# Kernel optimization log

Measured on AMD Instinct MI355X. Metric: run time of the kernel, lower is better.

Reference implementation:

```python
import jax, jax.numpy as jnp
import numpy as np

B, N, E, L, H, FA = 64, 29, 812, 9, 256, 5  # batch, max atoms, edges, layers, hidden, atom types
SCALE = 15.0


def _scatter_add(vals, idx):
    # vals [B,E,D], idx [B,E] -> [B,N,D]  (replaces one-hot multiply + reduce_sum)
    return jax.vmap(lambda v, i: jnp.zeros((N, v.shape[-1]), v.dtype).at[i].add(v))(vals, idx)


def _align(x, mask):
    n = jnp.sum(mask, axis=1, keepdims=True)
    mean = jnp.sum(x, axis=1, keepdims=True) / n
    return (x - mean) * mask


def setup_inputs() -> dict:
    key = jax.random.key(0)
    ks = iter(jax.random.split(key, 32))
    # fully connected edges i != j, same graph per batch element
    pairs = np.array([(i, j) for i in range(N) for j in range(N) if i != j], dtype=np.int32)
    edge_indices = jnp.tile(jnp.asarray(pairs)[None], (B, 1, 1))
    x_in = jax.random.normal(next(ks), (B, N, 3), jnp.float32)
    h_in = jax.random.normal(next(ks), (B, N, FA), jnp.float32)
    t = jax.random.uniform(next(ks), (B, N, 1), jnp.float32)
    node_mask = jnp.ones((B, N, 1), jnp.float32)
    edge_mask = jnp.ones((B, E, 1), jnp.float32)

    def w(k, shape, fan):
        return jax.random.normal(k, shape, jnp.float32) / np.float32(np.sqrt(fan))

    params = dict(
        win_w=w(next(ks), (FA + 1, H), FA + 1), win_b=jnp.zeros((H,), jnp.float32),
        wout_w=w(next(ks), (H, FA + 1), H), wout_b=jnp.zeros((FA + 1,), jnp.float32),
        e_w1=w(next(ks), (L, 2 * H + 2, H), 2 * H + 2), e_b1=jnp.zeros((L, H), jnp.float32),
        e_w2=w(next(ks), (L, H, H), H), e_b2=jnp.zeros((L, H), jnp.float32),
        att_w=w(next(ks), (L, H, 1), H), att_b=jnp.zeros((L, 1), jnp.float32),
        h_w1=w(next(ks), (L, 2 * H, H), 2 * H), h_b1=jnp.zeros((L, H), jnp.float32),
        h_w2=w(next(ks), (L, H, H), H), h_b2=jnp.zeros((L, H), jnp.float32),
        x_w1=w(next(ks), (L, 2 * H + 2, H), 2 * H + 2), x_b1=jnp.zeros((L, H), jnp.float32),
        x_w2=w(next(ks), (L, H, H), H), x_b2=jnp.zeros((L, H), jnp.float32),
        x_w3=w(next(ks), (L, H, 1), H),
    )
    return {"x_in": x_in, "h_in": h_in, "t": t, "node_mask": node_mask,
            "edge_mask": edge_mask, "edge_indices": edge_indices, **params}


def _forward(x_in, h_in, t, node_mask, edge_mask, edge_indices, p):
    bidx = jnp.arange(x_in.shape[0])[:, None]
    idx_i, idx_j = edge_indices[..., 0], edge_indices[..., 1]
    h = jnp.concatenate([h_in, t], axis=-1) @ p["win_w"] + p["win_b"]
    x = x_in
    # global pairwise distances, masked (the `a` feature)
    xi0, xj0 = x[bidx, idx_i], x[bidx, idx_j]
    a = jnp.sqrt(jnp.sum((xi0 - xj0) ** 2, axis=-1, keepdims=True)) * edge_mask
    for l in range(L):
        x_i, x_j = x[bidx, idx_i], x[bidx, idx_j]
        diff = (x_i - x_j) * edge_mask              # [B,E,3]
        d = jnp.sqrt(jnp.sum(diff ** 2, axis=-1, keepdims=True))
        h_i, h_j = h[bidx, idx_i], h[bidx, idx_j]
        feat = jnp.concatenate([h_i, h_j, d ** 2, a], axis=-1)  # [B,E,514]
        # --- update_x ---
        u = jax.nn.silu(feat @ p["x_w1"][l] + p["x_b1"][l])
        u = jax.nn.silu(u @ p["x_w2"][l] + p["x_b2"][l])
        u = jnp.tanh(u @ p["x_w3"][l]) * SCALE      # [B,E,1]
        u = u * diff / (d + 1.0)                    # [B,E,3]
        x = (x + _scatter_add(u, idx_i)) * node_mask
        # --- update_h ---
        m = jax.nn.silu(feat @ p["e_w1"][l] + p["e_b1"][l])
        m = jax.nn.silu(m @ p["e_w2"][l] + p["e_b2"][l])
        e = jax.nn.sigmoid(m @ p["att_w"][l] + p["att_b"][l])
        agg = _scatter_add(e * m, idx_i)            # [B,N,256]
        hm = jax.nn.silu(jnp.concatenate([h, agg], axis=-1) @ p["h_w1"][l] + p["h_b1"][l])
        hm = hm @ p["h_w2"][l] + p["h_b2"][l]
        h = (h + hm) * node_mask
    x_out = _align((x - x_in) * node_mask, node_mask)
    h_out = (h @ p["wout_w"] + p["wout_b"]) * node_mask
    return jnp.concatenate([x_out, h_out[..., :-1]], axis=-1)


def reference(x_in, h_in, t, node_mask, edge_mask, edge_indices,
              win_w, win_b, wout_w, wout_b,
              e_w1, e_b1, e_w2, e_b2, att_w, att_b,
              h_w1, h_b1, h_w2, h_b2,
              x_w1, x_b1, x_w2, x_b2, x_w3):
    p = dict(win_w=win_w, win_b=win_b, wout_w=wout_w, wout_b=wout_b,
             e_w1=e_w1, e_b1=e_b1, e_w2=e_w2, e_b2=e_b2,
             att_w=att_w, att_b=att_b,
             h_w1=h_w1, h_b1=h_b1, h_w2=h_w2, h_b2=h_b2,
             x_w1=x_w1, x_b1=x_b1, x_w2=x_w2, x_b2=x_b2, x_w3=x_w3)
    return _forward(x_in, h_in, t, node_mask, edge_mask, edge_indices, p)
```

## Files before the change

kernel.cpp:

```cpp
#include <hip/hip_runtime.h>
#include <math.h>

#define B_ 64
#define N_ 29
#define E_ 812
#define L_ 9
#define H_ 256
#define FA_ 5
#define BN_ (B_*N_)
#define BE_ (B_*E_)
#define DEG_ 28
#define SCALE_ 15.0f

typedef __attribute__((ext_vector_type(8))) short bf16x8;
typedef __attribute__((ext_vector_type(4))) float f32x4;

__device__ __forceinline__ float sigmoidf_(float v){ return 1.0f/(1.0f+expf(-v)); }
__device__ __forceinline__ float siluf_(float v){ return v/(1.0f+expf(-v)); }
__device__ __forceinline__ float fsilu_(float v){
    float e = __expf(-v);
    return v * __builtin_amdgcn_rcpf(1.0f + e);
}

__device__ __forceinline__ ushort f2bf(float f){
    uint u = __float_as_uint(f);
    u += 0x7fffu + ((u>>16)&1u);
    return (ushort)(u>>16);
}
__device__ __forceinline__ float bf2f(ushort h){ return __uint_as_float(((uint)h)<<16); }

__global__ void k_init_h(const float* __restrict__ h_in, const float* __restrict__ t,
                         const float* __restrict__ win_w, const float* __restrict__ win_b,
                         float* __restrict__ h)
{
    int node = blockIdx.x; int c = threadIdx.x;
    float in[6];
    #pragma unroll
    for (int k=0;k<FA_;k++) in[k] = h_in[node*FA_+k];
    in[5] = t[node];
    float acc = win_b[c];
    #pragma unroll
    for (int k=0;k<6;k++) acc += in[k]*win_w[k*H_+c];
    h[(size_t)node*H_+c] = acc;
}

__global__ void k_init_xa(const float* __restrict__ x_in, const int* __restrict__ eidx,
                          const float* __restrict__ emask, float* __restrict__ x, float* __restrict__ a)
{
    int gid = blockIdx.x*256 + threadIdx.x;
    if (gid < BN_*3) x[gid] = x_in[gid];
    if (gid < BE_) {
        int b = gid / E_;
        int ii = eidx[2*gid], jj = eidx[2*gid+1];
        const float* xi = x_in + (size_t)(b*N_+ii)*3;
        const float* xj = x_in + (size_t)(b*N_+jj)*3;
        float dx = xi[0]-xj[0], dy = xi[1]-xj[1], dz = xi[2]-xj[2];
        a[gid] = sqrtf(dx*dx+dy*dy+dz*dz) * emask[gid];
    }
}

__global__ void k_wprep(const float* __restrict__ xw2, const float* __restrict__ ew2,
                        ushort* __restrict__ WfU, ushort* __restrict__ WfM)
{
    int gid = blockIdx.x*256 + threadIdx.x;
    if (gid >= L_*2*8192) return;
    int lane = gid & 63;
    int rest = gid >> 6;
    int ct = rest & 15; rest >>= 4;
    int ks = rest & 7;  rest >>= 3;
    int p  = rest & 1;  int l = rest >> 1;
    const float* src = (p ? ew2 : xw2) + (size_t)l*H_*H_;
    ushort* dst = (p ? WfM : WfU) + (size_t)l*131072;
    int g = lane>>4, li = lane&15;
    int col = ct*16 + li;
    int kb  = ks*32 + g*8;
    size_t fo = ((size_t)(ks*16+ct)*64 + lane)*8;
    ushort* dh = dst + fo;
    ushort* dl = dst + 65536 + fo;
    #pragma unroll
    for (int j=0;j<8;j++){
        float v = src[(size_t)(kb+j)*H_ + col];
        ushort h = f2bf(v);
        dh[j] = h;
        dl[j] = f2bf(v - bf2f(h));
    }
}

struct GArg { const float* A; const float* Bw; const float* bias; const float* add; const float* rmask; float* C; };
struct GArgs { GArg g[6]; };

template<int ACT>
__global__ __launch_bounds__(256)
void k_gemm64(GArgs args, int M, int Kdim)
{
    const GArg ga = args.g[blockIdx.z];
    __shared__ float As[16*68];
    __shared__ float Bs[16*68];
    const int tid = threadIdx.x;
    const int row0 = blockIdx.x*64;
    const int col0 = blockIdx.y*64;
    const int ty = tid>>4, tx = tid&15;
    const int am = tid>>2, ak = (tid&3)<<2;
    const int bk = tid>>4, bn = (tid&15)<<2;
    float acc[4][4] = {};
    const float* Ap = ga.A + (size_t)min(row0+am, M-1)*Kdim + ak;
    const float* Bp = ga.Bw + (size_t)bk*H_ + col0 + bn;
    for (int k0=0; k0<Kdim; k0+=16) {
        float4 av = *(const float4*)(Ap + k0);
        float4 bv = *(const float4*)(Bp + (size_t)k0*H_);
        __syncthreads();
        As[(ak+0)*68+am]=av.x; As[(ak+1)*68+am]=av.y; As[(ak+2)*68+am]=av.z; As[(ak+3)*68+am]=av.w;
        *(float4*)&Bs[bk*68+bn] = bv;
        __syncthreads();
        #pragma unroll
        for (int k=0;k<16;k++) {
            float4 a4 = *(const float4*)&As[k*68 + (ty<<2)];
            float4 b4 = *(const float4*)&Bs[k*68 + (tx<<2)];
            float aa[4]={a4.x,a4.y,a4.z,a4.w};
            float bb[4]={b4.x,b4.y,b4.z,b4.w};
            #pragma unroll
            for (int i=0;i<4;i++)
                #pragma unroll
                for (int j=0;j<4;j++)
                    acc[i][j] = fmaf(aa[i], bb[j], acc[i][j]);
        }
    }
    const int r0 = row0 + (ty<<2);
    const int c0 = col0 + (tx<<2);
    float4 bias4 = make_float4(0.f,0.f,0.f,0.f);
    if (ga.bias) bias4 = *(const float4*)(ga.bias + c0);
    #pragma unroll
    for (int i=0;i<4;i++) {
        int r = r0+i;
        if (r >= M) break;
        float v0=acc[i][0]+bias4.x, v1=acc[i][1]+bias4.y, v2=acc[i][2]+bias4.z, v3=acc[i][3]+bias4.w;
        if (ga.add) {
            float4 ad = *(const float4*)(ga.add + (size_t)r*H_ + c0);
            v0+=ad.x; v1+=ad.y; v2+=ad.z; v3+=ad.w;
        }
        if (ACT==1) { v0=siluf_(v0); v1=siluf_(v1); v2=siluf_(v2); v3=siluf_(v3); }
        if (ga.rmask) { float mv = ga.rmask[r]; v0*=mv; v1*=mv; v2*=mv; v3*=mv; }
        *(float4*)(ga.C + (size_t)r*H_ + c0) = make_float4(v0,v1,v2,v3);
    }
}

__device__ __forceinline__ void frag_compute(
    const float* __restrict__ Xi, const float* __restrict__ Xj,
    const float* __restrict__ w5p, const float* __restrict__ w6p, const float* __restrict__ bp,
    int ni, int nj, float d2, float av, bool valid,
    int rt, int ks0, int lane,
    ushort (*fragH)[2][64][8], ushort (*fragL)[2][64][8])
{
    const int g = lane >> 4;
    if (valid){
        const float* xi = Xi + (size_t)ni*H_;
        const float* xj = Xj + (size_t)nj*H_;
        #pragma unroll
        for (int kq=0; kq<4; ++kq){
            int ks = ks0 + kq;
            int kb = ks*32 + g*8;
            float4 i0 = *(const float4*)(xi + kb),  i1 = *(const float4*)(xi + kb + 4);
            float4 j0 = *(const float4*)(xj + kb),  j1 = *(const float4*)(xj + kb + 4);
            float4 w50= *(const float4*)(w5p + kb), w51= *(const float4*)(w5p + kb + 4);
            float4 w60= *(const float4*)(w6p + kb), w61= *(const float4*)(w6p + kb + 4);
            float4 b0 = *(const float4*)(bp + kb),  b1v= *(const float4*)(bp + kb + 4);
            float v[8];
            v[0]=fsilu_(i0.x+j0.x+d2*w50.x+av*w60.x+b0.x);
            v[1]=fsilu_(i0.y+j0.y+d2*w50.y+av*w60.y+b0.y);
            v[2]=fsilu_(i0.z+j0.z+d2*w50.z+av*w60.z+b0.z);
            v[3]=fsilu_(i0.w+j0.w+d2*w50.w+av*w60.w+b0.w);
            v[4]=fsilu_(i1.x+j1.x+d2*w51.x+av*w61.x+b1v.x);
            v[5]=fsilu_(i1.y+j1.y+d2*w51.y+av*w61.y+b1v.y);
            v[6]=fsilu_(i1.z+j1.z+d2*w51.z+av*w61.z+b1v.z);
            v[7]=fsilu_(i1.w+j1.w+d2*w51.w+av*w61.w+b1v.w);
            ushort hh[8], ll[8];
            #pragma unroll
            for (int q=0;q<8;q++){ hh[q]=f2bf(v[q]); ll[q]=f2bf(v[q]-bf2f(hh[q])); }
            *(ushort4*)&fragH[ks][rt][lane][0] = make_ushort4(hh[0],hh[1],hh[2],hh[3]);
            *(ushort4*)&fragH[ks][rt][lane][4] = make_ushort4(hh[4],hh[5],hh[6],hh[7]);
            *(ushort4*)&fragL[ks][rt][lane][0] = make_ushort4(ll[0],ll[1],ll[2],ll[3]);
            *(ushort4*)&fragL[ks][rt][lane][4] = make_ushort4(ll[4],ll[5],ll[6],ll[7]);
        }
    } else {
        ushort4 z4 = make_ushort4(0,0,0,0);
        #pragma unroll
        for (int kq=0; kq<4; ++kq){
            int ks = ks0 + kq;
            *(ushort4*)&fragH[ks][rt][lane][0] = z4;
            *(ushort4*)&fragH[ks][rt][lane][4] = z4;
            *(ushort4*)&fragL[ks][rt][lane][0] = z4;
            *(ushort4*)&fragL[ks][rt][lane][4] = z4;
        }
    }
}

__device__ __forceinline__ void mfma_lds(
    const ushort (*fragH)[2][64][8], const ushort (*fragL)[2][64][8],
    const ushort* __restrict__ bp, int lane, f32x4 (&acc)[2][4])
{
    bf16x8 bh[2][4], bl[2][4];
    #pragma unroll
    for (int ct=0; ct<4; ++ct){
        bh[0][ct] = *(const bf16x8*)(bp + ct*512);
        bl[0][ct] = *(const bf16x8*)(bp + 65536 + ct*512);
    }
    #pragma unroll
    for (int ks=0; ks<8; ++ks){
        const int cur = ks & 1;
        const int nxt = cur ^ 1;
        if (ks < 7){
            #pragma unroll
            for (int ct=0; ct<4; ++ct){
                bh[nxt][ct] = *(const bf16x8*)(bp + (ks+1)*8192 + ct*512);
                bl[nxt][ct] = *(const bf16x8*)(bp + 65536 + (ks+1)*8192 + ct*512);
            }
        }
        bf16x8 ah[2], al[2];
        #pragma unroll
        for (int rt=0; rt<2; ++rt){
            ah[rt] = *(const bf16x8*)&fragH[ks][rt][lane][0];
            al[rt] = *(const bf16x8*)&fragL[ks][rt][lane][0];
        }
        #pragma unroll
        for (int ct=0; ct<4; ++ct){
            #pragma unroll
            for (int rt=0; rt<2; ++rt){
                acc[rt][ct] = __builtin_amdgcn_mfma_f32_16x16x32_bf16(ah[rt], bh[cur][ct], acc[rt][ct], 0,0,0);
                acc[rt][ct] = __builtin_amdgcn_mfma_f32_16x16x32_bf16(al[rt], bh[cur][ct], acc[rt][ct], 0,0,0);
                acc[rt][ct] = __builtin_amdgcn_mfma_f32_16x16x32_bf16(ah[rt], bl[cur][ct], acc[rt][ct], 0,0,0);
            }
        }
    }
}

__global__ __launch_bounds__(256, 4)
void k_edge_mega(const float* __restrict__ XHi, const float* __restrict__ XHj,
                 const float* __restrict__ EHi, const float* __restrict__ EHj,
                 const float* __restrict__ x_cur, const float* __restrict__ a,
                 const int* __restrict__ eidx, const float* __restrict__ emask,
                 const float* __restrict__ nmask,
                 const float* __restrict__ xw512, const float* __restrict__ xw513, const float* __restrict__ xb1,
                 const float* __restrict__ ew512, const float* __restrict__ ew513, const float* __restrict__ eb1,
                 const ushort* __restrict__ WfU, const ushort* __restrict__ WfM,
                 const float* __restrict__ xb2, const float* __restrict__ xw3,
                 const float* __restrict__ eb2, const float* __restrict__ attw,
                 const float* __restrict__ attb,
                 float* __restrict__ x_new, float* __restrict__ agg)
{
    __shared__ __align__(16) ushort fragH[8][2][64][8];
    __shared__ __align__(16) ushort fragL[8][2][64][8];
    __shared__ float pdLds[2][4][32];
    __shared__ float easLds[32];
    __shared__ float cxyz[DEG_][3];

    const int tid  = threadIdx.x;
    const int lane = tid & 63;
    const int wv   = tid >> 6;
    const int g    = lane >> 4;
    const int li   = lane & 15;
    const int rt   = wv & 1;
    const int ks0  = (wv >> 1)*4;
    const int n0   = blockIdx.x;

    const int frow = rt*16 + li;
    const bool valid = (frow < DEG_);
    int nj=0; float d2=0.f, av=0.f;
    if (valid){
        int bb = n0 / N_;
        size_t ge = (size_t)n0*DEG_ + frow;
        int jj = eidx[2*ge+1];
        nj = bb*N_ + jj;
        float em = emask[ge];
        float dx=(x_cur[n0*3+0]-x_cur[nj*3+0])*em;
        float dy=(x_cur[n0*3+1]-x_cur[nj*3+1])*em;
        float dz=(x_cur[n0*3+2]-x_cur[nj*3+2])*em;
        d2 = dx*dx+dy*dy+dz*dz;
        av = a[ge];
    }

    const ushort* bpU = WfU + ((size_t)(wv*4)*64 + lane)*8;
    const ushort* bpM = WfM + ((size_t)(wv*4)*64 + lane)*8;

    f32x4 acc[2][4];

    frag_compute(XHi, XHj, xw512, xw513, xb1, n0, nj, d2, av, valid, rt, ks0, lane, fragH, fragL);
    __syncthreads();

    #pragma unroll
    for (int r=0;r<2;++r)
        #pragma unroll
        for (int ct=0;ct<4;++ct)
            acc[r][ct] = (f32x4){0.f,0.f,0.f,0.f};
    mfma_lds(fragH, fragL, bpU, lane, acc);
    {
        float pdv[2][4];
        #pragma unroll
        for (int r=0;r<2;++r)
            #pragma unroll
            for (int rg=0;rg<4;++rg) pdv[r][rg]=0.f;
        #pragma unroll
        for (int ct=0; ct<4; ++ct){
            const int col = wv*64 + ct*16 + li;
            const float bi = xb2[col];
            const float wvv = xw3[col];
            #pragma unroll
            for (int r=0; r<2; ++r)
                #pragma unroll
                for (int rg=0; rg<4; ++rg)
                    pdv[r][rg] += fsilu_(acc[r][ct][rg] + bi)*wvv;
        }
        #pragma unroll
        for (int r=0;r<2;++r)
            #pragma unroll
            for (int rg=0;rg<4;++rg){
                float s = pdv[r][rg];
                s += __shfl_xor(s, 1, 16);
                s += __shfl_xor(s, 2, 16);
                s += __shfl_xor(s, 4, 16);
                s += __shfl_xor(s, 8, 16);
                if (li==0) pdLds[0][wv][r*16 + g*4 + rg] = s;
            }
    }
    __syncthreads();

    frag_compute(EHi, EHj, ew512, ew513, eb1, n0, nj, d2, av, valid, rt, ks0, lane, fragH, fragL);
    __syncthreads();

    #pragma unroll
    for (int r=0;r<2;++r)
        #pragma unroll
        for (int ct=0;ct<4;++ct)
            acc[r][ct] = (f32x4){0.f,0.f,0.f,0.f};
    mfma_lds(fragH, fragL, bpM, lane, acc);
    {
        float pdv[2][4];
        #pragma unroll
        for (int r=0;r<2;++r)
            #pragma unroll
            for (int rg=0;rg<4;++rg) pdv[r][rg]=0.f;
        #pragma unroll
        for (int ct=0; ct<4; ++ct){
            const int col = wv*64 + ct*16 + li;
            const float bi = eb2[col];
            const float wvv = attw[col];
            #pragma unroll
            for (int r=0; r<2; ++r)
                #pragma unroll
                for (int rg=0; rg<4; ++rg){
                    float v = fsilu_(acc[r][ct][rg] + bi);
                    acc[r][ct][rg] = v;
                    pdv[r][rg] += v*wvv;
                }
        }
        #pragma unroll
        for (int r=0;r<2;++r)
            #pragma unroll
            for (int rg=0;rg<4;++rg){
                float s = pdv[r][rg];
                s += __shfl_xor(s, 1, 16);
                s += __shfl_xor(s, 2, 16);
                s += __shfl_xor(s, 4, 16);
                s += __shfl_xor(s, 8, 16);
                if (li==0) pdLds[1][wv][r*16 + g*4 + rg] = s;
            }
    }
    __syncthreads();

    if (wv == 0){
        int t = lane;
        if (t < 32){
            float ea = 0.f;
            if (t < DEG_){
                float sU = pdLds[0][0][t]+pdLds[0][1][t]+pdLds[0][2][t]+pdLds[0][3][t];
                float sM = pdLds[1][0][t]+pdLds[1][1][t]+pdLds[1][2][t]+pdLds[1][3][t];
                float tsc = tanhf(sU)*SCALE_;
                ea = sigmoidf_(sM + attb[0]);
                size_t ge = (size_t)n0*DEG_ + t;
                int bb = n0 / N_;
                int jj = eidx[2*ge+1];
                int njs = bb*N_ + jj;
                float em = emask[ge];
                float dx=(x_cur[n0*3+0]-x_cur[njs*3+0])*em;
                float dy=(x_cur[n0*3+1]-x_cur[njs*3+1])*em;
                float dz=(x_cur[n0*3+2]-x_cur[njs*3+2])*em;
                float dd = sqrtf(dx*dx+dy*dy+dz*dz);
                float sc = tsc/(dd+1.0f);
                cxyz[t][0]=sc*dx; cxyz[t][1]=sc*dy; cxyz[t][2]=sc*dz;
            }
            easLds[t] = ea;
        }
        if (t == 0){
            float sx=0.f, sy=0.f, sz=0.f;
            #pragma unroll 4
            for (int k=0;k<DEG_;k++){ sx+=cxyz[k][0]; sy+=cxyz[k][1]; sz+=cxyz[k][2]; }
            float nm = nmask[n0];
            x_new[n0*3+0]=(x_cur[n0*3+0]+sx)*nm;
            x_new[n0*3+1]=(x_cur[n0*3+1]+sy)*nm;
            x_new[n0*3+2]=(x_cur[n0*3+2]+sz)*nm;
        }
    }
    __syncthreads();

    float p[4] = {0.f,0.f,0.f,0.f};
    #pragma unroll
    for (int r=0; r<2; ++r){
        #pragma unroll
        for (int rg=0; rg<4; ++rg){
            int row = r*16 + g*4 + rg;
            float w = easLds[row];
            #pragma unroll
            for (int ct=0; ct<4; ++ct)
                p[ct] += w*acc[r][ct][rg];
        }
    }
    #pragma unroll
    for (int ct=0; ct<4; ++ct){
        p[ct] += __shfl_xor(p[ct], 16);
        p[ct] += __shfl_xor(p[ct], 32);
    }
    if (g == 0){
        #pragma unroll
        for (int ct=0; ct<4; ++ct){
            int col = wv*64 + ct*16 + li;
            agg[(size_t)n0*H_ + col] = p[ct];
        }
    }
}

__global__ void k_out_x(const float* __restrict__ x, const float* __restrict__ x_in,
                        const float* __restrict__ nmask, float* __restrict__ out)
{
    int b = blockIdx.x; int l = threadIdx.x;
    int row = b*N_ + l;
    float xd0=0.f,xd1=0.f,xd2=0.f,nm=0.f;
    if (l < N_) {
        nm = nmask[row];
        xd0 = (x[(size_t)row*3+0]-x_in[(size_t)row*3+0])*nm;
        xd1 = (x[(size_t)row*3+1]-x_in[(size_t)row*3+1])*nm;
        xd2 = (x[(size_t)row*3+2]-x_in[(size_t)row*3+2])*nm;
    }
    float s0=xd0,s1=xd1,s2=xd2,sn=nm;
    #pragma unroll
    for (int off=32; off; off>>=1) {
        s0+=__shfl_xor(s0,off,64); s1+=__shfl_xor(s1,off,64);
        s2+=__shfl_xor(s2,off,64); sn+=__shfl_xor(sn,off,64);
    }
    float m0=s0/sn, m1=s1/sn, m2=s2/sn;
    if (l < N_) {
        out[(size_t)row*8+0]=(xd0-m0)*nm;
        out[(size_t)row*8+1]=(xd1-m1)*nm;
        out[(size_t)row*8+2]=(xd2-m2)*nm;
    }
}

__global__ void k_out_h(const float* __restrict__ h, const float* __restrict__ wout_w, const float* __restrict__ wout_b,
                        const float* __restrict__ nmask, float* __restrict__ out)
{
    int row = blockIdx.x; int lane = threadIdx.x;
    int c4 = lane<<2;
    float4 hv = *(const float4*)(h + (size_t)row*H_ + c4);
    float p0=0,p1=0,p2=0,p3=0,p4=0;
    float hvv[4] = {hv.x,hv.y,hv.z,hv.w};
    #pragma unroll
    for (int j=0;j<4;j++) {
        int k = c4+j;
        float hval = hvv[j];
        p0 += hval * wout_w[k*6+0];
        p1 += hval * wout_w[k*6+1];
        p2 += hval * wout_w[k*6+2];
        p3 += hval * wout_w[k*6+3];
        p4 += hval * wout_w[k*6+4];
    }
    #pragma unroll
    for (int off=32; off; off>>=1) {
        p0+=__shfl_xor(p0,off,64); p1+=__shfl_xor(p1,off,64); p2+=__shfl_xor(p2,off,64);
        p3+=__shfl_xor(p3,off,64); p4+=__shfl_xor(p4,off,64);
    }
    if (lane==0) {
        float nm = nmask[row];
        out[(size_t)row*8+3] = (p0+wout_b[0])*nm;
        out[(size_t)row*8+4] = (p1+wout_b[1])*nm;
        out[(size_t)row*8+5] = (p2+wout_b[2])*nm;
        out[(size_t)row*8+6] = (p3+wout_b[3])*nm;
        out[(size_t)row*8+7] = (p4+wout_b[4])*nm;
    }
}

extern "C" void kernel_launch(void* const* d_in, const int* in_sizes, int n_in,
                              void* d_out, int out_size, void* d_ws, size_t ws_size,
                              hipStream_t stream)
{
    const float* x_in  = (const float*)d_in[0];
    const float* h_in  = (const float*)d_in[1];
    const float* t     = (const float*)d_in[2];
    const float* nmask = (const float*)d_in[3];
    const float* emask = (const float*)d_in[4];
    const int*   eidx  = (const int*)d_in[5];
    const float* win_w = (const float*)d_in[6];
    const float* win_b = (const float*)d_in[7];
    const float* wout_w= (const float*)d_in[8];
    const float* wout_b= (const float*)d_in[9];
    const float* e_w1  = (const float*)d_in[10];
    const float* e_b1  = (const float*)d_in[11];
    const float* e_w2  = (const float*)d_in[12];
    const float* e_b2  = (const float*)d_in[13];
    const float* att_w = (const float*)d_in[14];
    const float* att_b = (const float*)d_in[15];
    const float* h_w1  = (const float*)d_in[16];
    const float* h_b1  = (const float*)d_in[17];
    const float* h_w2  = (const float*)d_in[18];
    const float* h_b2  = (const float*)d_in[19];
    const float* x_w1  = (const float*)d_in[20];
    const float* x_b1  = (const float*)d_in[21];
    const float* x_w2  = (const float*)d_in[22];
    const float* x_b2  = (const float*)d_in[23];
    const float* x_w3  = (const float*)d_in[24];
    float* out = (float*)d_out;

    char* ws = (char*)d_ws;
    size_t off = 0;
    auto alloc = [&](size_t bytes)->float* {
        float* p = (float*)(ws + off);
        off = (off + bytes + 255) & ~(size_t)255;
        return p;
    };
    float* h    = alloc((size_t)BN_*H_*4);
    float* xA   = alloc((size_t)BN_*3*4);
    float* xB   = alloc((size_t)BN_*3*4);
    float* a    = alloc((size_t)BE_*4);
    float* NB5  = alloc((size_t)5*BN_*H_*4);
    float* agg  = alloc((size_t)BN_*H_*4);
    float* hm1  = alloc((size_t)BN_*H_*4);
    ushort* WfU = (ushort*)alloc((size_t)L_*131072*sizeof(ushort));
    ushort* WfM = (ushort*)alloc((size_t)L_*131072*sizeof(ushort));

    k_init_h<<<BN_, H_, 0, stream>>>(h_in, t, win_w, win_b, h);
    k_init_xa<<<(BE_+255)/256, 256, 0, stream>>>(x_in, eidx, emask, xA, a);
    k_wprep<<<(L_*2*8192+255)/256, 256, 0, stream>>>(x_w2, e_w2, WfU, WfM);

    float* x_cur = xA;
    float* x_new = xB;

    for (int l=0; l<L_; l++) {
        const float* xw1l = x_w1 + (size_t)l*514*H_;
        const float* ew1l = e_w1 + (size_t)l*514*H_;
        const float* hw1l = h_w1 + (size_t)l*512*H_;

        GArgs na = {};
        const float* Bz[5] = { xw1l, xw1l+(size_t)256*H_, ew1l, ew1l+(size_t)256*H_, hw1l };
        for (int z=0;z<5;z++){
            na.g[z].A=h; na.g[z].Bw=Bz[z]; na.g[z].bias=nullptr; na.g[z].add=nullptr;
            na.g[z].rmask=nullptr; na.g[z].C=NB5 + (size_t)z*BN_*H_;
        }
        k_gemm64<0><<<dim3(BN_/64, H_/64, 5),256,0,stream>>>(na, BN_, H_);

        float* XHi=NB5;
        float* XHj=NB5+(size_t)BN_*H_;
        float* EHi=NB5+(size_t)2*BN_*H_;
        float* EHj=NB5+(size_t)3*BN_*H_;
        float* Htop=NB5+(size_t)4*BN_*H_;

        k_edge_mega<<<BN_, 256, 0, stream>>>(XHi, XHj, EHi, EHj, x_cur, a,
            eidx, emask, nmask,
            xw1l+(size_t)512*H_, xw1l+(size_t)513*H_, x_b1+(size_t)l*H_,
            ew1l+(size_t)512*H_, ew1l+(size_t)513*H_, e_b1+(size_t)l*H_,
            WfU + (size_t)l*131072, WfM + (size_t)l*131072,
            x_b2+(size_t)l*H_, x_w3+(size_t)l*H_,
            e_b2+(size_t)l*H_, att_w+(size_t)l*H_, att_b+l,
            x_new, agg);

        GArgs ha = {};
        ha.g[0] = { agg, hw1l+(size_t)256*H_, h_b1+(size_t)l*H_, Htop, nullptr, hm1 };
        k_gemm64<1><<<dim3(BN_/64,H_/64,1),256,0,stream>>>(ha, BN_, H_);

        GArgs h2 = {};
        h2.g[0] = { hm1, h_w2+(size_t)l*H_*H_, h_b2+(size_t)l*H_, h, nmask, h };
        k_gemm64<0><<<dim3(BN_/64,H_/64,1),256,0,stream>>>(h2, BN_, H_);

        float* tmp = x_cur; x_cur = x_new; x_new = tmp;
    }

    k_out_x<<<B_,64,0,stream>>>(x_cur, x_in, nmask, out);
    k_out_h<<<BN_,64,0,stream>>>(h, wout_w, wout_b, nmask, out);
}
```

Before: 1.171 ms.

## Replace FP32 SIMT node GEMMs with split-bf16x3 MFMA GEMMs on pre-swizzled fragments

Replaces the scalar-FMA 64x64-tiled node GEMMs (the per-layer h projections and the two h-update GEMMs) with an MFMA kernel. Operands are held as three bf16 planes (hi/mid/lo) and six cross products are accumulated to approximate FP32 precision. Activations (h, agg, hm1) are now written by their producer kernels directly in the MFMA fragment layout, and a new prep kernel pre-swizzles all seven weight blocks per layer. This targets the FP32 ALU cost of the node GEMMs, at the cost of extra conversion work in the epilogues and a much lower block count per launch (one 64-row band per block).

```diff
diff --git a/kernel.cpp b/kernel.cpp
--- a/kernel.cpp
+++ b/kernel.cpp
@@ -10,6 +10,7 @@
 #define BN_ (B_*N_)
 #define BE_ (B_*E_)
 #define DEG_ 28
+#define NBAND_ (BN_/64)
 #define SCALE_ 15.0f
 
 typedef __attribute__((ext_vector_type(8))) short bf16x8;
@@ -29,9 +30,20 @@
 }
 __device__ __forceinline__ float bf2f(ushort h){ return __uint_as_float(((uint)h)<<16); }
 
+__device__ __forceinline__ void store3(ushort* __restrict__ p0, ushort* __restrict__ p1,
+                                       ushort* __restrict__ p2, int row, int c, float v){
+    int band=row>>6, r=row&63, rt=r>>4, li=r&15;
+    int ks=c>>5, rem=c&31, gg=rem>>3, j=rem&7;
+    size_t fo = (((size_t)((band*8+ks)*4+rt)*64)+(gg*16+li))*8+j;
+    ushort h0=f2bf(v); float r1=v-bf2f(h0);
+    ushort h1=f2bf(r1); float r2=r1-bf2f(h1);
+    p0[fo]=h0; p1[fo]=h1; p2[fo]=f2bf(r2);
+}
+
 __global__ void k_init_h(const float* __restrict__ h_in, const float* __restrict__ t,
                          const float* __restrict__ win_w, const float* __restrict__ win_b,
-                         float* __restrict__ h)
+                         float* __restrict__ h,
+                         ushort* __restrict__ hp0, ushort* __restrict__ hp1, ushort* __restrict__ hp2)
 {
     int node = blockIdx.x; int c = threadIdx.x;
     float in[6];
@@ -42,6 +54,7 @@
     #pragma unroll
     for (int k=0;k<6;k++) acc += in[k]*win_w[k*H_+c];
     h[(size_t)node*H_+c] = acc;
+    store3(hp0, hp1, hp2, node, c, acc);
 }
 
 __global__ void k_init_xa(const float* __restrict__ x_in, const int* __restrict__ eidx,
@@ -86,61 +99,115 @@
     }
 }
 
-struct GArg { const float* A; const float* Bw; const float* bias; const float* add; const float* rmask; float* C; };
-struct GArgs { GArg g[6]; };
-
-template<int ACT>
-__global__ __launch_bounds__(256)
-void k_gemm64(GArgs args, int M, int Kdim)
-{
-    const GArg ga = args.g[blockIdx.z];
-    __shared__ float As[16*68];
-    __shared__ float Bs[16*68];
-    const int tid = threadIdx.x;
-    const int row0 = blockIdx.x*64;
-    const int col0 = blockIdx.y*64;
-    const int ty = tid>>4, tx = tid&15;
-    const int am = tid>>2, ak = (tid&3)<<2;
-    const int bk = tid>>4, bn = (tid&15)<<2;
-    float acc[4][4] = {};
-    const float* Ap = ga.A + (size_t)min(row0+am, M-1)*Kdim + ak;
-    const float* Bp = ga.Bw + (size_t)bk*H_ + col0 + bn;
-    for (int k0=0; k0<Kdim; k0+=16) {
-        float4 av = *(const float4*)(Ap + k0);
-        float4 bv = *(const float4*)(Bp + (size_t)k0*H_);
-        __syncthreads();
-        As[(ak+0)*68+am]=av.x; As[(ak+1)*68+am]=av.y; As[(ak+2)*68+am]=av.z; As[(ak+3)*68+am]=av.w;
-        *(float4*)&Bs[bk*68+bn] = bv;
-        __syncthreads();
-        #pragma unroll
-        for (int k=0;k<16;k++) {
-            float4 a4 = *(const float4*)&As[k*68 + (ty<<2)];
-            float4 b4 = *(const float4*)&Bs[k*68 + (tx<<2)];
-            float aa[4]={a4.x,a4.y,a4.z,a4.w};
-            float bb[4]={b4.x,b4.y,b4.z,b4.w};
-            #pragma unroll
-            for (int i=0;i<4;i++)
-                #pragma unroll
-                for (int j=0;j<4;j++)
-                    acc[i][j] = fmaf(aa[i], bb[j], acc[i][j]);
-        }
-    }
-    const int r0 = row0 + (ty<<2);
-    const int c0 = col0 + (tx<<2);
-    float4 bias4 = make_float4(0.f,0.f,0.f,0.f);
-    if (ga.bias) bias4 = *(const float4*)(ga.bias + c0);
-    #pragma unroll
-    for (int i=0;i<4;i++) {
-        int r = r0+i;
-        if (r >= M) break;
-        float v0=acc[i][0]+bias4.x, v1=acc[i][1]+bias4.y, v2=acc[i][2]+bias4.z, v3=acc[i][3]+bias4.w;
-        if (ga.add) {
-            float4 ad = *(const float4*)(ga.add + (size_t)r*H_ + c0);
-            v0+=ad.x; v1+=ad.y; v2+=ad.z; v3+=ad.w;
-        }
-        if (ACT==1) { v0=siluf_(v0); v1=siluf_(v1); v2=siluf_(v2); v3=siluf_(v3); }
-        if (ga.rmask) { float mv = ga.rmask[r]; v0*=mv; v1*=mv; v2*=mv; v3*=mv; }
-        *(float4*)(ga.C + (size_t)r*H_ + c0) = make_float4(v0,v1,v2,v3);
+__global__ void k_wprep6(const float* __restrict__ xw1, const float* __restrict__ ew1,
+                         const float* __restrict__ hw1, const float* __restrict__ hw2,
+                         ushort* __restrict__ Wf6)
+{
+    int gid = blockIdx.x*256 + threadIdx.x;
+    if (gid >= L_*7*8192) return;
+    int lane = gid & 63;
+    int rest = gid >> 6;
+    int ct = rest & 15; rest >>= 4;
+    int ks = rest & 7;  rest >>= 3;
+    int m  = rest % 7;  int l = rest / 7;
+    const float* src;
+    switch (m) {
+        case 0: src = xw1 + (size_t)l*514*H_; break;
+        case 1: src = xw1 + (size_t)l*514*H_ + (size_t)256*H_; break;
+        case 2: src = ew1 + (size_t)l*514*H_; break;
+        case 3: src = ew1 + (size_t)l*514*H_ + (size_t)256*H_; break;
+        case 4: src = hw1 + (size_t)l*512*H_; break;
+        case 5: src = hw1 + (size_t)l*512*H_ + (size_t)256*H_; break;
+        default: src = hw2 + (size_t)l*H_*H_; break;
+    }
+    ushort* dst = Wf6 + (size_t)(l*7+m)*196608;
+    int g = lane>>4, li = lane&15;
+    int col = ct*16 + li;
+    int kb  = ks*32 + g*8;
+    size_t fo = ((size_t)(ks*16+ct)*64 + lane)*8;
+    #pragma unroll
+    for (int j=0;j<8;j++){
+        float v = src[(size_t)(kb+j)*H_ + col];
+        ushort h0 = f2bf(v); float r1 = v - bf2f(h0);
+        ushort h1 = f2bf(r1); float r2 = r1 - bf2f(h1);
+        dst[fo+j] = h0;
+        dst[65536+fo+j] = h1;
+        dst[131072+fo+j] = f2bf(r2);
+    }
+}
+
+struct NArg6 { const ushort* A0; const ushort* A1; const ushort* A2;
+               const ushort* Wf; const float* bias; const float* addf; const float* rmask;
+               float* Cf; ushort* C0; ushort* C1; ushort* C2; int act; };
+struct NArgs6 { NArg6 g[5]; };
+
+__global__ __launch_bounds__(256, 2)
+void k_ngemm6(NArgs6 args)
+{
+    const NArg6 ga = args.g[blockIdx.z];
+    const int tid  = threadIdx.x;
+    const int lane = tid & 63;
+    const int wv   = tid >> 6;
+    const int g    = lane >> 4;
+    const int li   = lane & 15;
+    const int band = blockIdx.x;
+    const int row0 = band*64;
+
+    const size_t abase = (size_t)band*16384 + (size_t)lane*8;
+    const ushort* bp = ga.Wf + ((size_t)(wv*4)*64 + lane)*8;
+
+    f32x4 acc[4][4];
+    #pragma unroll
+    for (int rt=0;rt<4;++rt)
+        #pragma unroll
+        for (int ct=0;ct<4;++ct)
+            acc[rt][ct] = (f32x4){0.f,0.f,0.f,0.f};
+
+    #pragma unroll
+    for (int ks=0; ks<8; ++ks){
+        bf16x8 a0[4], a1[4], a2[4];
+        #pragma unroll
+        for (int rt=0; rt<4; ++rt){
+            size_t o = abase + (size_t)(ks*4+rt)*512;
+            a0[rt] = *(const bf16x8*)(ga.A0 + o);
+            a1[rt] = *(const bf16x8*)(ga.A1 + o);
+            a2[rt] = *(const bf16x8*)(ga.A2 + o);
+        }
+        #pragma unroll
+        for (int ct=0; ct<4; ++ct){
+            bf16x8 b0 = *(const bf16x8*)(bp + ks*8192 + ct*512);
+            bf16x8 b1 = *(const bf16x8*)(bp + 65536 + ks*8192 + ct*512);
+            bf16x8 b2 = *(const bf16x8*)(bp + 131072 + ks*8192 + ct*512);
+            #pragma unroll
+            for (int rt=0; rt<4; ++rt){
+                acc[rt][ct] = __builtin_amdgcn_mfma_f32_16x16x32_bf16(a0[rt], b0, acc[rt][ct], 0,0,0);
+                acc[rt][ct] = __builtin_amdgcn_mfma_f32_16x16x32_bf16(a1[rt], b0, acc[rt][ct], 0,0,0);
+                acc[rt][ct] = __builtin_amdgcn_mfma_f32_16x16x32_bf16(a0[rt], b1, acc[rt][ct], 0,0,0);
+                acc[rt][ct] = __builtin_amdgcn_mfma_f32_16x16x32_bf16(a1[rt], b1, acc[rt][ct], 0,0,0);
+                acc[rt][ct] = __builtin_amdgcn_mfma_f32_16x16x32_bf16(a2[rt], b0, acc[rt][ct], 0,0,0);
+                acc[rt][ct] = __builtin_amdgcn_mfma_f32_16x16x32_bf16(a0[rt], b2, acc[rt][ct], 0,0,0);
+            }
+        }
+    }
+
+    #pragma unroll
+    for (int ct=0; ct<4; ++ct){
+        const int col = wv*64 + ct*16 + li;
+        const float bi = ga.bias ? ga.bias[col] : 0.f;
+        #pragma unroll
+        for (int rt=0; rt<4; ++rt){
+            #pragma unroll
+            for (int rg=0; rg<4; ++rg){
+                int row = row0 + rt*16 + g*4 + rg;
+                float v = acc[rt][ct][rg] + bi;
+                size_t o = (size_t)row*H_ + col;
+                if (ga.addf)  v += ga.addf[o];
+                if (ga.act)   v  = siluf_(v);
+                if (ga.rmask) v *= ga.rmask[row];
+                if (ga.Cf) ga.Cf[o] = v;
+                if (ga.C0) store3(ga.C0, ga.C1, ga.C2, row, col, v);
+            }
+        }
     }
 }
 
@@ -245,7 +312,8 @@
                  const float* __restrict__ xb2, const float* __restrict__ xw3,
                  const float* __restrict__ eb2, const float* __restrict__ attw,
                  const float* __restrict__ attb,
-                 float* __restrict__ x_new, float* __restrict__ agg)
+                 float* __restrict__ x_new,
+                 ushort* __restrict__ aggp0, ushort* __restrict__ aggp1, ushort* __restrict__ aggp2)
 {
     __shared__ __align__(16) ushort fragH[8][2][64][8];
     __shared__ __align__(16) ushort fragL[8][2][64][8];
@@ -422,7 +490,7 @@
         #pragma unroll
         for (int ct=0; ct<4; ++ct){
             int col = wv*64 + ct*16 + li;
-            agg[(size_t)n0*H_ + col] = p[ct];
+            store3(aggp0, aggp1, aggp2, n0, col, p[ct]);
         }
     }
 }
@@ -524,19 +592,29 @@
         off = (off + bytes + 255) & ~(size_t)255;
         return p;
     };
-    float* h    = alloc((size_t)BN_*H_*4);
-    float* xA   = alloc((size_t)BN_*3*4);
-    float* xB   = alloc((size_t)BN_*3*4);
-    float* a    = alloc((size_t)BE_*4);
-    float* NB5  = alloc((size_t)5*BN_*H_*4);
-    float* agg  = alloc((size_t)BN_*H_*4);
-    float* hm1  = alloc((size_t)BN_*H_*4);
-    ushort* WfU = (ushort*)alloc((size_t)L_*131072*sizeof(ushort));
-    ushort* WfM = (ushort*)alloc((size_t)L_*131072*sizeof(ushort));
-
-    k_init_h<<<BN_, H_, 0, stream>>>(h_in, t, win_w, win_b, h);
+    const size_t PLANE = (size_t)NBAND_*16384;
+    float*  h     = alloc((size_t)BN_*H_*4);
+    ushort* hp0   = (ushort*)alloc(PLANE*2);
+    ushort* hp1   = (ushort*)alloc(PLANE*2);
+    ushort* hp2   = (ushort*)alloc(PLANE*2);
+    float*  xA    = alloc((size_t)BN_*3*4);
+    float*  xB    = alloc((size_t)BN_*3*4);
+    float*  a     = alloc((size_t)BE_*4);
+    float*  NB5   = alloc((size_t)5*BN_*H_*4);
+    ushort* aggp0 = (ushort*)alloc(PLANE*2);
+    ushort* aggp1 = (ushort*)alloc(PLANE*2);
+    ushort* aggp2 = (ushort*)alloc(PLANE*2);
+    ushort* hm1p0 = (ushort*)alloc(PLANE*2);
+    ushort* hm1p1 = (ushort*)alloc(PLANE*2);
+    ushort* hm1p2 = (ushort*)alloc(PLANE*2);
+    ushort* WfU   = (ushort*)alloc((size_t)L_*131072*sizeof(ushort));
+    ushort* WfM   = (ushort*)alloc((size_t)L_*131072*sizeof(ushort));
+    ushort* Wf6   = (ushort*)alloc((size_t)L_*7*196608*sizeof(ushort));
+
+    k_init_h<<<BN_, H_, 0, stream>>>(h_in, t, win_w, win_b, h, hp0, hp1, hp2);
     k_init_xa<<<(BE_+255)/256, 256, 0, stream>>>(x_in, eidx, emask, xA, a);
     k_wprep<<<(L_*2*8192+255)/256, 256, 0, stream>>>(x_w2, e_w2, WfU, WfM);
+    k_wprep6<<<(L_*7*8192+255)/256, 256, 0, stream>>>(x_w1, e_w1, h_w1, h_w2, Wf6);
 
     float* x_cur = xA;
     float* x_new = xB;
@@ -544,21 +622,24 @@
     for (int l=0; l<L_; l++) {
         const float* xw1l = x_w1 + (size_t)l*514*H_;
         const float* ew1l = e_w1 + (size_t)l*514*H_;
-        const float* hw1l = h_w1 + (size_t)l*512*H_;
-
-        GArgs na = {};
-        const float* Bz[5] = { xw1l, xw1l+(size_t)256*H_, ew1l, ew1l+(size_t)256*H_, hw1l };
-        for (int z=0;z<5;z++){
-            na.g[z].A=h; na.g[z].Bw=Bz[z]; na.g[z].bias=nullptr; na.g[z].add=nullptr;
-            na.g[z].rmask=nullptr; na.g[z].C=NB5 + (size_t)z*BN_*H_;
-        }
-        k_gemm64<0><<<dim3(BN_/64, H_/64, 5),256,0,stream>>>(na, BN_, H_);
+        const ushort* Wl6 = Wf6 + (size_t)l*7*196608;
 
         float* XHi=NB5;
         float* XHj=NB5+(size_t)BN_*H_;
         float* EHi=NB5+(size_t)2*BN_*H_;
         float* EHj=NB5+(size_t)3*BN_*H_;
         float* Htop=NB5+(size_t)4*BN_*H_;
+
+        NArgs6 na = {};
+        for (int z=0; z<5; z++){
+            na.g[z].A0=hp0; na.g[z].A1=hp1; na.g[z].A2=hp2;
+            na.g[z].Wf = Wl6 + (size_t)z*196608;
+            na.g[z].bias=nullptr; na.g[z].addf=nullptr; na.g[z].rmask=nullptr;
+            na.g[z].Cf = NB5 + (size_t)z*BN_*H_;
+            na.g[z].C0=nullptr; na.g[z].C1=nullptr; na.g[z].C2=nullptr;
+            na.g[z].act=0;
+        }
+        k_ngemm6<<<dim3(NBAND_,1,5),256,0,stream>>>(na);
 
         k_edge_mega<<<BN_, 256, 0, stream>>>(XHi, XHj, EHi, EHj, x_cur, a,
             eidx, emask, nmask,
@@ -567,15 +648,23 @@
             WfU + (size_t)l*131072, WfM + (size_t)l*131072,
             x_b2+(size_t)l*H_, x_w3+(size_t)l*H_,
             e_b2+(size_t)l*H_, att_w+(size_t)l*H_, att_b+l,
-            x_new, agg);
-
-        GArgs ha = {};
-        ha.g[0] = { agg, hw1l+(size_t)256*H_, h_b1+(size_t)l*H_, Htop, nullptr, hm1 };
-        k_gemm64<1><<<dim3(BN_/64,H_/64,1),256,0,stream>>>(ha, BN_, H_);
-
-        GArgs h2 = {};
-        h2.g[0] = { hm1, h_w2+(size_t)l*H_*H_, h_b2+(size_t)l*H_, h, nmask, h };
-        k_gemm64<0><<<dim3(BN_/64,H_/64,1),256,0,stream>>>(h2, BN_, H_);
+            x_new, aggp0, aggp1, aggp2);
+
+        NArgs6 ha = {};
+        ha.g[0].A0=aggp0; ha.g[0].A1=aggp1; ha.g[0].A2=aggp2;
+        ha.g[0].Wf = Wl6 + (size_t)5*196608;
+        ha.g[0].bias = h_b1+(size_t)l*H_; ha.g[0].addf = Htop; ha.g[0].rmask=nullptr;
+        ha.g[0].Cf=nullptr; ha.g[0].C0=hm1p0; ha.g[0].C1=hm1p1; ha.g[0].C2=hm1p2;
+        ha.g[0].act=1;
+        k_ngemm6<<<dim3(NBAND_,1,1),256,0,stream>>>(ha);
+
+        NArgs6 h2 = {};
+        h2.g[0].A0=hm1p0; h2.g[0].A1=hm1p1; h2.g[0].A2=hm1p2;
+        h2.g[0].Wf = Wl6 + (size_t)6*196608;
+        h2.g[0].bias = h_b2+(size_t)l*H_; h2.g[0].addf = h; h2.g[0].rmask=nmask;
+        h2.g[0].Cf=h; h2.g[0].C0=hp0; h2.g[0].C1=hp1; h2.g[0].C2=hp2;
+        h2.g[0].act=0;
+        k_ngemm6<<<dim3(NBAND_,1,1),256,0,stream>>>(h2);
 
         float* tmp = x_cur; x_cur = x_new; x_new = tmp;
     }
```

Result: slower. 1.701 ms (+45.2%).

## Run per-layer node projection GEMMs on MFMA with three-way bf16 split

Applied to the files above, without the earlier changes.

Replaces the FP32 SIMT tiled GEMM that projects h through five weight slices each layer with an MFMA bf16 kernel. Both h and the weights are split into three bf16 planes to keep near-FP32 accuracy, using six MFMA products per tile. Weights are pre-swizzled once into fragment layout, and h is re-split into fragment planes every layer by a new kernel. This adds one launch per layer, extra global traffic for the planes, and six times the MFMA work, in exchange for much higher matrix throughput than FP32 FMA.

```diff
diff --git a/kernel.cpp b/kernel.cpp
--- a/kernel.cpp
+++ b/kernel.cpp
@@ -10,6 +10,7 @@
 #define BN_ (B_*N_)
 #define BE_ (B_*E_)
 #define DEG_ 28
+#define NBAND_ (BN_/64)
 #define SCALE_ 15.0f
 
 typedef __attribute__((ext_vector_type(8))) short bf16x8;
@@ -84,6 +85,66 @@
         dh[j] = h;
         dl[j] = f2bf(v - bf2f(h));
     }
+}
+
+__global__ void k_wprep6(const float* __restrict__ xw1, const float* __restrict__ ew1,
+                         const float* __restrict__ hw1, ushort* __restrict__ Wf6)
+{
+    int gid = blockIdx.x*256 + threadIdx.x;
+    if (gid >= L_*5*8192) return;
+    int lane = gid & 63;
+    int rest = gid >> 6;
+    int ct = rest & 15; rest >>= 4;
+    int ks = rest & 7;  rest >>= 3;
+    int m  = rest % 5;  int l = rest / 5;
+    const float* src;
+    switch (m) {
+        case 0: src = xw1 + (size_t)l*514*H_; break;
+        case 1: src = xw1 + (size_t)l*514*H_ + (size_t)256*H_; break;
+        case 2: src = ew1 + (size_t)l*514*H_; break;
+        case 3: src = ew1 + (size_t)l*514*H_ + (size_t)256*H_; break;
+        default: src = hw1 + (size_t)l*512*H_; break;
+    }
+    ushort* dst = Wf6 + (size_t)(l*5+m)*196608;
+    int g = lane>>4, li = lane&15;
+    int col = ct*16 + li;
+    int kb  = ks*32 + g*8;
+    size_t fo = ((size_t)(ks*16+ct)*64 + lane)*8;
+    #pragma unroll
+    for (int j=0;j<8;j++){
+        float v = src[(size_t)(kb+j)*H_ + col];
+        ushort h0 = f2bf(v); float r1 = v - bf2f(h0);
+        ushort h1 = f2bf(r1); float r2 = r1 - bf2f(h1);
+        dst[fo+j] = h0;
+        dst[65536+fo+j] = h1;
+        dst[131072+fo+j] = f2bf(r2);
+    }
+}
+
+__global__ void k_hfrag(const float* __restrict__ h,
+                        ushort* __restrict__ p0, ushort* __restrict__ p1, ushort* __restrict__ p2)
+{
+    int gid = blockIdx.x*256 + threadIdx.x;
+    if (gid >= BN_*32) return;
+    int row = gid >> 5, octet = gid & 31;
+    const float* src = h + (size_t)row*H_ + octet*8;
+    int band=row>>6, r=row&63, rt=r>>4, li=r&15;
+    int ks=octet>>2, gg=octet&3;
+    size_t fo = (((size_t)((band*8+ks)*4+rt)*64)+(gg*16+li))*8;
+    ushort q0[8], q1[8], q2[8];
+    #pragma unroll
+    for (int j=0;j<8;j++){
+        float v = src[j];
+        ushort h0 = f2bf(v); float r1 = v - bf2f(h0);
+        ushort h1 = f2bf(r1); float r2 = r1 - bf2f(h1);
+        q0[j]=h0; q1[j]=h1; q2[j]=f2bf(r2);
+    }
+    *(ushort4*)(p0+fo)   = make_ushort4(q0[0],q0[1],q0[2],q0[3]);
+    *(ushort4*)(p0+fo+4) = make_ushort4(q0[4],q0[5],q0[6],q0[7]);
+    *(ushort4*)(p1+fo)   = make_ushort4(q1[0],q1[1],q1[2],q1[3]);
+    *(ushort4*)(p1+fo+4) = make_ushort4(q1[4],q1[5],q1[6],q1[7]);
+    *(ushort4*)(p2+fo)   = make_ushort4(q2[0],q2[1],q2[2],q2[3]);
+    *(ushort4*)(p2+fo+4) = make_ushort4(q2[4],q2[5],q2[6],q2[7]);
 }
 
 struct GArg { const float* A; const float* Bw; const float* bias; const float* add; const float* rmask; float* C; };
@@ -141,6 +202,65 @@
         if (ACT==1) { v0=siluf_(v0); v1=siluf_(v1); v2=siluf_(v2); v3=siluf_(v3); }
         if (ga.rmask) { float mv = ga.rmask[r]; v0*=mv; v1*=mv; v2*=mv; v3*=mv; }
         *(float4*)(ga.C + (size_t)r*H_ + c0) = make_float4(v0,v1,v2,v3);
+    }
+}
+
+struct NArg6 { const ushort* A0; const ushort* A1; const ushort* A2;
+               const ushort* Wf; float* Cf; };
+struct NArgs6 { NArg6 g[5]; };
+
+__global__ __launch_bounds__(256, 4)
+void k_ngemm6(NArgs6 args)
+{
+    const NArg6 ga = args.g[blockIdx.z];
+    const int tid  = threadIdx.x;
+    const int lane = tid & 63;
+    const int wv   = tid >> 6;
+    const int g    = lane >> 4;
+    const int li   = lane & 15;
+    const int band = blockIdx.x;
+    const int row0 = band*64;
+    const int ctg  = blockIdx.y*4 + wv;
+
+    const size_t abase = (size_t)band*16384 + (size_t)lane*8;
+    const ushort* bp = ga.Wf + (size_t)ctg*512 + (size_t)lane*8;
+
+    f32x4 acc[4];
+    #pragma unroll
+    for (int rt=0;rt<4;++rt) acc[rt] = (f32x4){0.f,0.f,0.f,0.f};
+
+    #pragma unroll
+    for (int ks=0; ks<8; ++ks){
+        bf16x8 a0[4], a1[4], a2[4];
+        #pragma unroll
+        for (int rt=0; rt<4; ++rt){
+            size_t o = abase + (size_t)(ks*4+rt)*512;
+            a0[rt] = *(const bf16x8*)(ga.A0 + o);
+            a1[rt] = *(const bf16x8*)(ga.A1 + o);
+            a2[rt] = *(const bf16x8*)(ga.A2 + o);
+        }
+        bf16x8 b0 = *(const bf16x8*)(bp + ks*8192);
+        bf16x8 b1 = *(const bf16x8*)(bp + 65536 + ks*8192);
+        bf16x8 b2 = *(const bf16x8*)(bp + 131072 + ks*8192);
+        #pragma unroll
+        for (int rt=0; rt<4; ++rt){
+            acc[rt] = __builtin_amdgcn_mfma_f32_16x16x32_bf16(a0[rt], b0, acc[rt], 0,0,0);
+            acc[rt] = __builtin_amdgcn_mfma_f32_16x16x32_bf16(a1[rt], b0, acc[rt], 0,0,0);
+            acc[rt] = __builtin_amdgcn_mfma_f32_16x16x32_bf16(a0[rt], b1, acc[rt], 0,0,0);
+            acc[rt] = __builtin_amdgcn_mfma_f32_16x16x32_bf16(a1[rt], b1, acc[rt], 0,0,0);
+            acc[rt] = __builtin_amdgcn_mfma_f32_16x16x32_bf16(a2[rt], b0, acc[rt], 0,0,0);
+            acc[rt] = __builtin_amdgcn_mfma_f32_16x16x32_bf16(a0[rt], b2, acc[rt], 0,0,0);
+        }
+    }
+
+    const int col = ctg*16 + li;
+    #pragma unroll
+    for (int rt=0; rt<4; ++rt){
+        #pragma unroll
+        for (int rg=0; rg<4; ++rg){
+            int row = row0 + rt*16 + g*4 + rg;
+            ga.Cf[(size_t)row*H_ + col] = acc[rt][rg];
+        }
     }
 }
 
@@ -524,19 +644,25 @@
         off = (off + bytes + 255) & ~(size_t)255;
         return p;
     };
-    float* h    = alloc((size_t)BN_*H_*4);
-    float* xA   = alloc((size_t)BN_*3*4);
-    float* xB   = alloc((size_t)BN_*3*4);
-    float* a    = alloc((size_t)BE_*4);
-    float* NB5  = alloc((size_t)5*BN_*H_*4);
-    float* agg  = alloc((size_t)BN_*H_*4);
-    float* hm1  = alloc((size_t)BN_*H_*4);
-    ushort* WfU = (ushort*)alloc((size_t)L_*131072*sizeof(ushort));
-    ushort* WfM = (ushort*)alloc((size_t)L_*131072*sizeof(ushort));
+    const size_t PLANE = (size_t)NBAND_*16384;
+    float*  h     = alloc((size_t)BN_*H_*4);
+    ushort* hp0   = (ushort*)alloc(PLANE*2);
+    ushort* hp1   = (ushort*)alloc(PLANE*2);
+    ushort* hp2   = (ushort*)alloc(PLANE*2);
+    float*  xA    = alloc((size_t)BN_*3*4);
+    float*  xB    = alloc((size_t)BN_*3*4);
+    float*  a     = alloc((size_t)BE_*4);
+    float*  NB5   = alloc((size_t)5*BN_*H_*4);
+    float*  agg   = alloc((size_t)BN_*H_*4);
+    float*  hm1   = alloc((size_t)BN_*H_*4);
+    ushort* WfU   = (ushort*)alloc((size_t)L_*131072*sizeof(ushort));
+    ushort* WfM   = (ushort*)alloc((size_t)L_*131072*sizeof(ushort));
+    ushort* Wf6   = (ushort*)alloc((size_t)L_*5*196608*sizeof(ushort));
 
     k_init_h<<<BN_, H_, 0, stream>>>(h_in, t, win_w, win_b, h);
     k_init_xa<<<(BE_+255)/256, 256, 0, stream>>>(x_in, eidx, emask, xA, a);
     k_wprep<<<(L_*2*8192+255)/256, 256, 0, stream>>>(x_w2, e_w2, WfU, WfM);
+    k_wprep6<<<(L_*5*8192+255)/256, 256, 0, stream>>>(x_w1, e_w1, h_w1, Wf6);
 
     float* x_cur = xA;
     float* x_new = xB;
@@ -545,20 +671,23 @@
         const float* xw1l = x_w1 + (size_t)l*514*H_;
         const float* ew1l = e_w1 + (size_t)l*514*H_;
         const float* hw1l = h_w1 + (size_t)l*512*H_;
-
-        GArgs na = {};
-        const float* Bz[5] = { xw1l, xw1l+(size_t)256*H_, ew1l, ew1l+(size_t)256*H_, hw1l };
-        for (int z=0;z<5;z++){
-            na.g[z].A=h; na.g[z].Bw=Bz[z]; na.g[z].bias=nullptr; na.g[z].add=nullptr;
-            na.g[z].rmask=nullptr; na.g[z].C=NB5 + (size_t)z*BN_*H_;
-        }
-        k_gemm64<0><<<dim3(BN_/64, H_/64, 5),256,0,stream>>>(na, BN_, H_);
+        const ushort* Wl6 = Wf6 + (size_t)l*5*196608;
 
         float* XHi=NB5;
         float* XHj=NB5+(size_t)BN_*H_;
         float* EHi=NB5+(size_t)2*BN_*H_;
         float* EHj=NB5+(size_t)3*BN_*H_;
         float* Htop=NB5+(size_t)4*BN_*H_;
+
+        k_hfrag<<<(BN_*32+255)/256, 256, 0, stream>>>(h, hp0, hp1, hp2);
+
+        NArgs6 na = {};
+        for (int z=0; z<5; z++){
+            na.g[z].A0=hp0; na.g[z].A1=hp1; na.g[z].A2=hp2;
+            na.g[z].Wf = Wl6 + (size_t)z*196608;
+            na.g[z].Cf = NB5 + (size_t)z*BN_*H_;
+        }
+        k_ngemm6<<<dim3(NBAND_,4,5),256,0,stream>>>(na);
 
         k_edge_mega<<<BN_, 256, 0, stream>>>(XHi, XHj, EHi, EHj, x_cur, a,
             eidx, emask, nmask,
```

Result: no change. 1.155 ms, median of 2 (-1.4%).
